# Optimization experiments

Hardware: AMD Instinct MI355X
Metric: run time of the kernel (lower is better)

## Reference

```python
import jax, jax.numpy as jnp
import numpy as np

DEPTH = 8
IN_FEATURES = 512
OUT_FEATURES = 256
LEAF_COUNT = 2 ** DEPTH          # 256
GATE_COUNT = LEAF_COUNT - 1      # 255
BATCH = 65536


def setup_inputs() -> dict:
    key = jax.random.key(0)
    k1, k2, k3 = jax.random.split(key, 3)
    x = jax.random.normal(k1, (BATCH, IN_FEATURES), dtype=jnp.float32)
    # gw stored transposed as (in_features, gate_count), kaiming-like scale
    gw = jax.random.normal(k2, (IN_FEATURES, GATE_COUNT), dtype=jnp.float32) * (1.0 / np.sqrt(IN_FEATURES))
    gb = jnp.zeros((GATE_COUNT,), dtype=jnp.float32)
    z = jax.random.normal(k3, (OUT_FEATURES, LEAF_COUNT), dtype=jnp.float32)
    return {"x": x, "gw": gw, "gb": gb, "z": z}


def _leaf_probs(x, gw, gb):
    # gatings: (B, gate_count); node it's left child (2p+1) uses g, right child (2p+2) uses 1-g
    g = jax.nn.sigmoid(x @ gw + gb)
    B = x.shape[0]
    dens = jnp.ones((B, 1), dtype=x.dtype)
    for d in range(DEPTH):  # level-wise vectorized traversal, O(depth) steps
        lo, hi = 2 ** d - 1, 2 ** (d + 1) - 1
        gl = g[:, lo:hi]  # (B, 2^d) gatings at this level
        # interleave [parent*g, parent*(1-g)] -> children order matches heap layout
        dens = jnp.stack([dens * gl, dens * (1.0 - gl)], axis=-1).reshape(B, -1)
    return dens  # (B, leaf_count)


def reference(x, gw, gb, z):
    leaf = _leaf_probs(x, gw, gb)        # (B, L)
    # constant projection: z @ leaf_probs^T, then transpose -> (B, out)
    return leaf @ z.T
```

## Files before the change

### kernel.cpp

```cpp
#include <hip/hip_runtime.h>
#include <hip/hip_bf16.h>
#include <stdint.h>


typedef short bf16x8 __attribute__((ext_vector_type(8)));
typedef float f32x4  __attribute__((ext_vector_type(4)));

__device__ __forceinline__ unsigned short f2bf(float f) {
    union { float f; uint32_t u; } c; c.f = f;
    uint32_t u = c.u;
    return (unsigned short)((u + 0x7FFFu + ((u >> 16) & 1u)) >> 16);
}

__device__ __forceinline__ uint32_t pkbf(float a, float b) {
    union { __hip_bfloat162 h; uint32_t u; } cv;
    cv.h = __float22bfloat162_rn(make_float2(a, b));
    return cv.u;
}

__global__ __launch_bounds__(256) void softtree_prep(
    const float* __restrict__ gw, const float* __restrict__ z,
    unsigned short* __restrict__ gwt, unsigned short* __restrict__ zb)
{
    if (blockIdx.x < 32) {
        __shared__ float tsm[64][65];
        const int k0 = (blockIdx.x >> 2) * 64;
        const int n0 = (blockIdx.x & 3) * 64;
        const int r = threadIdx.x >> 6;
        const int c = threadIdx.x & 63;
        const int n = n0 + c;
        #pragma unroll
        for (int i = 0; i < 16; ++i) {
            int kk = r + i * 4;
            tsm[kk][c] = (n < 255) ? gw[(size_t)(k0 + kk) * 255 + n] : 0.0f;
        }
        __syncthreads();
        #pragma unroll
        for (int i = 0; i < 16; ++i) {
            int nn = r + i * 4;
            gwt[(size_t)(n0 + nn) * 512 + k0 + c] = f2bf(tsm[c][nn]);
        }
    } else {
        int base = (blockIdx.x - 32) * 1024 + threadIdx.x * 4;
        const float4 v = *(const float4*)(z + base);
        ushort4 o;
        o.x = f2bf(v.x); o.y = f2bf(v.y); o.z = f2bf(v.z); o.w = f2bf(v.w);
        *(ushort4*)(zb + base) = o;
    }
}

__global__ __launch_bounds__(512, 4) void softtree_main(
    const float* __restrict__ x, const float* __restrict__ gb,
    const unsigned short* __restrict__ gwt, const unsigned short* __restrict__ zb,
    float* __restrict__ out)
{
    __shared__ char smraw[81920];
    float* gs = (float*)smraw;

    const int tid  = threadIdx.x;
    const int lane = tid & 63;
    const int wv   = tid >> 6;
    const int q    = lane >> 4;
    const int l15  = lane & 15;
    const int wr   = wv & 3;
    const int wc   = wv >> 2;
    const int R0   = blockIdx.x * 128;

    float gbv[8];
    #pragma unroll
    for (int nt = 0; nt < 8; ++nt) {
        int col = 128 * wc + nt * 16 + l15;
        gbv[nt] = (col < 255) ? gb[col] : 0.0f;
    }
    asm volatile("s_waitcnt vmcnt(0)" ::: "memory");

    const float* xsrc0 = x + (size_t)(R0 + 16 * wv + (lane >> 3)) * 512
                           + (size_t)(((lane & 7) ^ (lane >> 3)) * 4);
    const unsigned short* gsrc0 = gwt + (size_t)(32 * wv + (lane >> 2)) * 512
                                      + (size_t)(((lane & 3) ^ ((lane >> 2) & 3)) * 8);
    const uint32_t xdst = (uint32_t)wv * 2048;
    const uint32_t gdst = 49152u + (uint32_t)wv * 2048;

    #define ISSUE_X(kc, xb)                                                                    \
        do {                                                                                   \
            const float* s_ = xsrc0 + (kc) * 32;                                               \
            __builtin_amdgcn_global_load_lds(                                                  \
                (const __attribute__((address_space(1))) void*)(s_),                           \
                (__attribute__((address_space(3))) void*)(smraw + (xb) * 16384 + xdst),        \
                16, 0, 0);                                                                     \
            __builtin_amdgcn_global_load_lds(                                                  \
                (const __attribute__((address_space(1))) void*)(s_ + 8 * 512),                 \
                (__attribute__((address_space(3))) void*)(smraw + (xb) * 16384 + xdst + 1024), \
                16, 0, 0);                                                                     \
        } while (0)

    #define ISSUE_G(kc, gwb)                                                                   \
        do {                                                                                   \
            const unsigned short* s_ = gsrc0 + (kc) * 32;                                      \
            __builtin_amdgcn_global_load_lds(                                                  \
                (const __attribute__((address_space(1))) void*)(s_),                           \
                (__attribute__((address_space(3))) void*)(smraw + (gwb) * 16384 + gdst),       \
                16, 0, 0);                                                                     \
            __builtin_amdgcn_global_load_lds(                                                  \
                (const __attribute__((address_space(1))) void*)(s_ + 16 * 512),                \
                (__attribute__((address_space(3))) void*)(smraw + (gwb) * 16384 + gdst + 1024),\
                16, 0, 0);                                                                     \
        } while (0)

    f32x4 acc[2][8];
    #pragma unroll
    for (int t = 0; t < 2; ++t)
        #pragma unroll
        for (int i = 0; i < 8; ++i) acc[t][i] = (f32x4){0.f, 0.f, 0.f, 0.f};

    ISSUE_X(0, 0);
    ISSUE_G(0, 0);
    ISSUE_X(1, 1);

    int xb = 0, gwb = 0;
    for (int kc = 0; kc < 15; ++kc) {
        asm volatile("s_waitcnt vmcnt(2)" ::: "memory");
        __builtin_amdgcn_s_barrier();
        __builtin_amdgcn_sched_barrier(0);

        ISSUE_G(kc + 1, gwb ^ 1);
        if (kc < 14) {
            int xb2 = xb + 2; if (xb2 >= 3) xb2 -= 3;
            ISSUE_X(kc + 2, xb2);
        }

        {
            const char* xbase = smraw + xb * 16384;
            const char* gbase = smraw + 49152 + gwb * 16384;
            bf16x8 a[2];
            #pragma unroll
            for (int t = 0; t < 2; ++t) {
                const char* ra = xbase + (64 * t + 16 * wr + l15) * 128;
                f32x4 lo = *(const f32x4*)(ra + (((2 * q)     ^ (l15 & 7)) * 16));
                f32x4 hi = *(const f32x4*)(ra + (((2 * q + 1) ^ (l15 & 7)) * 16));
                union { bf16x8 v; uint32_t u[4]; } pk;
                pk.u[0] = pkbf(lo[0], lo[1]); pk.u[1] = pkbf(lo[2], lo[3]);
                pk.u[2] = pkbf(hi[0], hi[1]); pk.u[3] = pkbf(hi[2], hi[3]);
                a[t] = pk.v;
            }
            __builtin_amdgcn_s_setprio(1);
            #pragma unroll
            for (int nt = 0; nt < 8; ++nt) {
                const bf16x8 b = *(const bf16x8*)(gbase + (128 * wc + nt * 16 + l15) * 64
                                                        + ((q ^ (l15 & 3)) * 16));
                acc[0][nt] = __builtin_amdgcn_mfma_f32_16x16x32_bf16(a[0], b, acc[0][nt], 0, 0, 0);
                acc[1][nt] = __builtin_amdgcn_mfma_f32_16x16x32_bf16(a[1], b, acc[1][nt], 0, 0, 0);
            }
            __builtin_amdgcn_s_setprio(0);
        }

        xb = (xb == 2) ? 0 : xb + 1;
        gwb ^= 1;
    }

    asm volatile("s_waitcnt vmcnt(0)" ::: "memory");
    __builtin_amdgcn_s_barrier();
    __builtin_amdgcn_sched_barrier(0);
    {
        const char* xbase = smraw + xb * 16384;
        const char* gbase = smraw + 49152 + gwb * 16384;
        bf16x8 a[2];
        #pragma unroll
        for (int t = 0; t < 2; ++t) {
            const char* ra = xbase + (64 * t + 16 * wr + l15) * 128;
            f32x4 lo = *(const f32x4*)(ra + (((2 * q)     ^ (l15 & 7)) * 16));
            f32x4 hi = *(const f32x4*)(ra + (((2 * q + 1) ^ (l15 & 7)) * 16));
            union { bf16x8 v; uint32_t u[4]; } pk;
            pk.u[0] = pkbf(lo[0], lo[1]); pk.u[1] = pkbf(lo[2], lo[3]);
            pk.u[2] = pkbf(hi[0], hi[1]); pk.u[3] = pkbf(hi[2], hi[3]);
            a[t] = pk.v;
        }
        __builtin_amdgcn_s_setprio(1);
        #pragma unroll
        for (int nt = 0; nt < 8; ++nt) {
            const bf16x8 b = *(const bf16x8*)(gbase + (128 * wc + nt * 16 + l15) * 64
                                                    + ((q ^ (l15 & 3)) * 16));
            acc[0][nt] = __builtin_amdgcn_mfma_f32_16x16x32_bf16(a[0], b, acc[0][nt], 0, 0, 0);
            acc[1][nt] = __builtin_amdgcn_mfma_f32_16x16x32_bf16(a[1], b, acc[1][nt], 0, 0, 0);
        }
        __builtin_amdgcn_s_setprio(0);
    }

    #undef ISSUE_X
    #undef ISSUE_G

    for (int t = 0; t < 2; ++t) {
        __syncthreads();

        #pragma unroll
        for (int nt = 0; nt < 8; ++nt) {
            const int col = 128 * wc + nt * 16 + l15;
            #pragma unroll
            for (int r = 0; r < 4; ++r) {
                const int rowl = 16 * wr + 4 * q + r;
                float v = acc[t][nt][r] + gbv[nt];
                gs[rowl * 258 + col] = 1.0f / (1.0f + __expf(-v));
            }
        }
        __syncthreads();

        const float* gr = gs + (16 * wr + l15) * 258;
        float g0v = gr[0];
        float t1v[2] = { g0v, 1.0f - g0v };
        float t2v[4], t3v[8];
        #pragma unroll
        for (int u = 0; u < 2; ++u) {
            float gl = gr[1 + u];
            t2v[2 * u] = t1v[u] * gl; t2v[2 * u + 1] = t1v[u] - t2v[2 * u];
        }
        #pragma unroll
        for (int u = 0; u < 4; ++u) {
            float gl = gr[3 + u];
            t3v[2 * u] = t2v[u] * gl; t3v[2 * u + 1] = t2v[u] - t3v[2 * u];
        }
        bf16x8 a2[8];
        #pragma unroll
        for (int c = 0; c < 8; ++c) {
            const int G = c * 4 + q;
            float p = t3v[c];
            float g3 = gr[7 + c];
            p = (q & 2) ? (p - p * g3) : (p * g3);
            float g4 = gr[15 + 2 * c + (q >> 1)];
            p = (q & 1) ? (p - p * g4) : (p * g4);
            float g5 = gr[31 + G];
            float a0 = p * g5, a1 = p - a0;
            float g6a = gr[63 + 2 * G], g6b = gr[64 + 2 * G];
            float b00 = a0 * g6a, b01 = a0 - b00;
            float b10 = a1 * g6b, b11 = a1 - b10;
            float g70 = gr[127 + 4 * G], g71 = gr[128 + 4 * G];
            float g72 = gr[129 + 4 * G], g73 = gr[130 + 4 * G];
            float lf0 = b00 * g70, lf1 = b00 - lf0;
            float lf2 = b01 * g71, lf3 = b01 - lf2;
            float lf4 = b10 * g72, lf5 = b10 - lf4;
            float lf6 = b11 * g73, lf7 = b11 - lf6;
            union { bf16x8 v; uint32_t u[4]; } pk;
            pk.u[0] = pkbf(lf0, lf1);
            pk.u[1] = pkbf(lf2, lf3);
            pk.u[2] = pkbf(lf4, lf5);
            pk.u[3] = pkbf(lf6, lf7);
            a2[c] = pk.v;
        }

        f32x4 acc2[8];
        #pragma unroll
        for (int i = 0; i < 8; ++i) acc2[i] = (f32x4){0.f, 0.f, 0.f, 0.f};
        __builtin_amdgcn_s_setprio(1);
        #pragma unroll
        for (int nt = 0; nt < 8; ++nt) {
            const unsigned short* zrow = zb + (size_t)(128 * wc + nt * 16 + l15) * 256 + q * 8;
            #pragma unroll
            for (int c = 0; c < 8; ++c) {
                bf16x8 b = *(const bf16x8*)(zrow + c * 32);
                acc2[nt] = __builtin_amdgcn_mfma_f32_16x16x32_bf16(a2[c], b, acc2[nt], 0, 0, 0);
            }
        }
        __builtin_amdgcn_s_setprio(0);

        #pragma unroll
        for (int nt = 0; nt < 8; ++nt) {
            const int col = 128 * wc + nt * 16 + l15;
            #pragma unroll
            for (int r = 0; r < 4; ++r) {
                const int row = R0 + t * 64 + 16 * wr + 4 * q + r;
                out[(size_t)row * 256 + col] = acc2[nt][r];
            }
        }
    }
}

extern "C" void kernel_launch(void* const* d_in, const int* in_sizes, int n_in,
                              void* d_out, int out_size, void* d_ws, size_t ws_size,
                              hipStream_t stream) {
    const float* x  = (const float*)d_in[0];
    const float* gw = (const float*)d_in[1];
    const float* gb = (const float*)d_in[2];
    const float* z  = (const float*)d_in[3];
    float* outp = (float*)d_out;

    unsigned short* gwt = (unsigned short*)d_ws;
    unsigned short* zbf = gwt + 256 * 512;

    softtree_prep<<<96, 256, 0, stream>>>(gw, z, gwt, zbf);
    softtree_main<<<512, 512, 0, stream>>>(x, gb, gwt, zbf, outp);
}
```

Baseline: 284.6 us.

## Split fused gating GEMM and tree/projection into two kernels

The single fused kernel becomes two. The first computes the sigmoid gatings and writes them to global memory, using the output buffer as scratch. The second reads each 64-row tile of gatings back into padded shared memory, then runs the tree traversal and the leaf projection, writing the result in place. This separates the two phases so each kernel can have its own register and shared-memory budget and scheduling. The cost is an extra full write and read of a B×256 float intermediate plus a second launch.

```diff
diff --git a/kernel.cpp b/kernel.cpp
--- a/kernel.cpp
+++ b/kernel.cpp
@@ -49,13 +49,11 @@
     }
 }
 
-__global__ __launch_bounds__(512, 4) void softtree_main(
+__global__ __launch_bounds__(512, 4) void softtree_g(
     const float* __restrict__ x, const float* __restrict__ gb,
-    const unsigned short* __restrict__ gwt, const unsigned short* __restrict__ zb,
-    float* __restrict__ out)
+    const unsigned short* __restrict__ gwt, float* __restrict__ g)
 {
     __shared__ char smraw[81920];
-    float* gs = (float*)smraw;
 
     const int tid  = threadIdx.x;
     const int lane = tid & 63;
@@ -189,22 +187,51 @@
     #undef ISSUE_X
     #undef ISSUE_G
 
+    #pragma unroll
     for (int t = 0; t < 2; ++t) {
-        __syncthreads();
-
         #pragma unroll
         for (int nt = 0; nt < 8; ++nt) {
             const int col = 128 * wc + nt * 16 + l15;
             #pragma unroll
             for (int r = 0; r < 4; ++r) {
-                const int rowl = 16 * wr + 4 * q + r;
+                const int row = R0 + t * 64 + 16 * wr + 4 * q + r;
                 float v = acc[t][nt][r] + gbv[nt];
-                gs[rowl * 258 + col] = 1.0f / (1.0f + __expf(-v));
-            }
+                g[(size_t)row * 256 + col] = 1.0f / (1.0f + __expf(-v));
+            }
+        }
+    }
+}
+
+__global__ __launch_bounds__(512, 4) void softtree_tree(
+    const float* __restrict__ g, const unsigned short* __restrict__ zb,
+    float* __restrict__ out)
+{
+    __shared__ float gs[64 * 260];
+
+    const int tid  = threadIdx.x;
+    const int lane = tid & 63;
+    const int wv   = tid >> 6;
+    const int q    = lane >> 4;
+    const int l15  = lane & 15;
+    const int wr   = wv & 3;
+    const int wc   = wv >> 2;
+    const int R0   = blockIdx.x * 128;
+
+    const int srow = tid >> 3;
+    const int scol = (tid & 7) * 32;
+
+    for (int t = 0; t < 2; ++t) {
+        if (t) __syncthreads();
+
+        const float* gsrc = g + (size_t)(R0 + 64 * t + srow) * 256 + scol;
+        #pragma unroll
+        for (int i = 0; i < 8; ++i) {
+            f32x4 v = *(const f32x4*)(gsrc + 4 * i);
+            *(f32x4*)(gs + srow * 260 + scol + 4 * i) = v;
         }
         __syncthreads();
 
-        const float* gr = gs + (16 * wr + l15) * 258;
+        const float* gr = gs + (16 * wr + l15) * 260;
         float g0v = gr[0];
         float t1v[2] = { g0v, 1.0f - g0v };
         float t2v[4], t3v[8];
@@ -286,5 +313,6 @@
     unsigned short* zbf = gwt + 256 * 512;
 
     softtree_prep<<<96, 256, 0, stream>>>(gw, z, gwt, zbf);
-    softtree_main<<<512, 512, 0, stream>>>(x, gb, gwt, zbf, outp);
-}
+    softtree_g<<<512, 512, 0, stream>>>(x, gb, gwt, outp);
+    softtree_tree<<<512, 512, 0, stream>>>(outp, zbf, outp);
+}
```

After: 300.9 us. +5.7%, slower.
